# Kernel optimization log

Hardware: AMD Instinct MI355X
Metric: run time of the kernel (lower is better)

The kernel has to match this reference:

```python
import jax, jax.numpy as jnp
import numpy as np

M = 16384          # test points
N = 16384          # train points
D = 2              # (kx, ky)
CHUNK = 8192       # rows of K_star per chunk (matches torch default)


def setup_inputs() -> dict:
    key = jax.random.key(0)
    k1, k2, k3 = jax.random.split(key, 3)
    X_test = jax.random.normal(k1, (M, D), dtype=jnp.float32)
    X_train = jax.random.normal(k2, (N, D), dtype=jnp.float32)
    alpha = jax.random.normal(k3, (N, 2), dtype=jnp.float32)  # dual vars [Re, Im]
    log_lengthscale = jnp.asarray(np.log(0.1), dtype=jnp.float32)
    log_outputscale = jnp.asarray(np.log(1.0), dtype=jnp.float32)
    return {
        "X_test": X_test,
        "X_train": X_train,
        "alpha": alpha,
        "log_lengthscale": log_lengthscale,
        "log_outputscale": log_outputscale,
    }


def reference(X_test, X_train, alpha, log_lengthscale, log_outputscale):
    """Posterior mean mu* = K_rbf(X_test, X_train) @ alpha, chunked over test rows."""
    ell2 = jnp.exp(log_lengthscale) ** 2
    sf2 = jnp.exp(log_outputscale) ** 2
    xt_sq = jnp.sum(X_train * X_train, axis=1)  # (N,)

    def chunk_fn(xc):  # xc: (CHUNK, D)
        # squared euclidean distances (clamped at 0 for numerical safety)
        sq = (jnp.sum(xc * xc, axis=1)[:, None]
              + xt_sq[None, :]
              - 2.0 * (xc @ X_train.T))          # (CHUNK, N)
        sq = jnp.maximum(sq, 0.0)
        K = sf2 * jnp.exp(-0.5 * sq / ell2)      # RBF kernel values
        return K @ alpha                          # (CHUNK, 2)

    m = X_test.shape[0]
    chunks = X_test.reshape(m // CHUNK, CHUNK, D)
    out = jax.lax.map(chunk_fn, chunks)           # (m//CHUNK, CHUNK, 2)
    return out.reshape(m, 2)
```

## Files before the change

### kernel.cpp

```cpp
#include <hip/hip_runtime.h>
#include <math.h>

#define M_PTS 16384
#define N_PTS 16384

#define NC 42
#define NCELLS (NC * NC)
#define H 0.25f
#define INV_H 4.0f
#define ORIG (-5.25f)
#define TCUT 20.0f
#define KMAX 7
#define MAXROWS 16
#define NWAVES (M_PTS / 64)
#define CHUNK 1024
#define MAX_ITEMS 4096

#define OFF_NITEMS 0
#define OFF_TRCUR 64
#define OFF_TECUR (OFF_TRCUR + NCELLS * 4)
#define OFF_SROW  (OFF_TECUR + NCELLS * 4)
#define OFF_SPRE  (OFF_SROW + NWAVES * MAXROWS * 4)
#define OFF_ITEMS (OFF_SPRE + NWAVES * (MAXROWS + 1) * 4)
#define OFF_TRA   ((OFF_ITEMS + MAX_ITEMS * 4 + 255) & ~255)
#define OFF_TRW1  (OFF_TRA + N_PTS * 16)
#define OFF_T4    (OFF_TRW1 + N_PTS * 4)
#define WS_NEED   (OFF_T4 + (size_t)M_PTS * 16)

__device__ __forceinline__ float fexp2(float x) {
#if __has_builtin(__builtin_amdgcn_exp2f)
    return __builtin_amdgcn_exp2f(x);
#else
    return exp2f(x);
#endif
}

__device__ __forceinline__ void gatomic_fadd(float* p, float v) {
    asm volatile("global_atomic_add_f32 %0, %1, off" :: "v"(p), "v"(v) : "memory");
}

__device__ __forceinline__ int cellco(float v) {
    int c = (int)floorf((v - ORIG) * INV_H);
    return min(NC - 1, max(0, c));
}

__global__ __launch_bounds__(1024) void prep_kernel(
        const float2* __restrict__ Xtr, const float2* __restrict__ Xte,
        const float* __restrict__ log_ell,
        int* __restrict__ trcur, int* __restrict__ tecur,
        int* __restrict__ sRowG, int* __restrict__ sPreG,
        int* __restrict__ items, int* __restrict__ nitemsG) {
    __shared__ int hTr[NCELLS], hTe[NCELLS];
    __shared__ int trsL[NCELLS + 1], PL[NCELLS + 1];
    __shared__ int wz[16];
    const int tid = threadIdx.x;
    const int lane = tid & 63;
    const int wid = tid >> 6;

    if (tid == 0) nitemsG[0] = 0;
    for (int i = tid; i < NCELLS; i += 1024) { hTr[i] = 0; hTe[i] = 0; }
    __syncthreads();
    for (int i = tid; i < N_PTS; i += 1024) {
        float2 t = Xtr[i];
        atomicAdd(&hTr[cellco(t.y) * NC + cellco(t.x)], 1);
        float2 x = Xte[i];
        atomicAdd(&hTe[cellco(x.y) * NC + cellco(x.x)], 1);
    }
    __syncthreads();

    {
        const int grp = tid >> 9;
        const int t = tid & 511;
        int* __restrict__ h  = grp ? hTe : hTr;
        int* __restrict__ s  = grp ? PL : trsL;
        int* __restrict__ cg = grp ? tecur : trcur;

        int lo[4];
        int sum = 0;
        const bool act = (t < 441);
#pragma unroll
        for (int k = 0; k < 4; ++k) {
            int c = t * 4 + k;
            int v = act ? h[c] : 0;
            lo[k] = sum; sum += v;
        }
        int inc = sum;
#pragma unroll
        for (int d = 1; d < 64; d <<= 1) {
            int u = __shfl_up(inc, d, 64);
            if (lane >= d) inc += u;
        }
        if (lane == 63) wz[wid] = inc;
        __syncthreads();
        int base = 0;
        const int w0 = grp << 3;
        for (int w = w0; w < wid; ++w) base += wz[w];
        int ex = base + inc - sum;
        if (act) {
#pragma unroll
            for (int k = 0; k < 4; ++k) {
                int c = t * 4 + k;
                int v = ex + lo[k];
                s[c] = v;
                cg[c] = v;
            }
        }
        if (tid == 0) { trsL[NCELLS] = N_PTS; PL[NCELLS] = N_PTS; }
    }
    __syncthreads();

    if (tid < NWAVES) {
        const int w = tid;
        const float ell = expf(log_ell[0]);
        const float cmag = 0.5f / (ell * ell) * 1.4426950408889634f;
        const float r2 = TCUT / cmag;
        const int K = (int)floorf(sqrtf(r2) * INV_H) + 1;

        int clo, chi;
        {
            int s = w * 64, lo = 0, hi = NCELLS;
            while (lo + 1 < hi) { int m = (lo + hi) >> 1; if (PL[m] <= s) lo = m; else hi = m; }
            clo = lo;
            s = w * 64 + 63; lo = 0; hi = NCELLS;
            while (lo + 1 < hi) { int m = (lo + hi) >> 1; if (PL[m] <= s) lo = m; else hi = m; }
            chi = lo;
        }
        const int rl = clo / NC, cl = clo % NC;
        const int rh = chi / NC, ch = chi % NC;
        int wlo = max(0, rl - K), whi = min(NC - 1, rh + K);
        int nr = whi - wlo + 1;
        bool full = (K > KMAX) || (nr > MAXROWS);

        int pre = 0;
        if (full) {
            sRowG[w * MAXROWS] = 0;
            sPreG[w * (MAXROWS + 1)] = 0;
            pre = N_PTS;
            for (int i = 1; i <= MAXROWS; ++i) sPreG[w * (MAXROWS + 1) + i] = N_PTS;
        } else {
            const bool single = (rl == rh);
            const int cmin = single ? cl : 0;
            const int cmax = single ? ch : (NC - 1);
            sPreG[w * (MAXROWS + 1)] = 0;
            int idx = 0;
            for (int wr = wlo; wr <= whi; ++wr, ++idx) {
                int dy = (wr < rl) ? (rl - wr) : ((wr > rh) ? (wr - rh) : 0);
                int kx;
                if (dy <= 1) kx = K;
                else {
                    float d = (float)(dy - 1) * H;
                    kx = (int)floorf(sqrtf(fmaxf(r2 - d * d, 0.f)) * INV_H) + 1;
                }
                int c0 = max(0, cmin - kx);
                int c1 = min(NC - 1, cmax + kx);
                int js = trsL[wr * NC + c0];
                int je = trsL[wr * NC + c1 + 1];
                sRowG[w * MAXROWS + idx] = js - pre;
                pre += je - js;
                sPreG[w * (MAXROWS + 1) + idx + 1] = pre;
            }
            for (; idx < MAXROWS; ++idx)
                sPreG[w * (MAXROWS + 1) + idx + 1] = pre;
        }
        const int nch = (pre + CHUNK - 1) / CHUNK;
        for (int k = 0; k < nch; ++k) {
            int slot = atomicAdd(nitemsG, 1);
            items[slot] = w | (k << 16);
        }
    }
}

__global__ void scatter_kernel(const float2* __restrict__ Xtr,
                               const float2* __restrict__ Xte,
                               const float2* __restrict__ alpha,
                               const float* __restrict__ log_ell,
                               const float* __restrict__ log_sf,
                               int* __restrict__ trcur, int* __restrict__ tecur,
                               float4* __restrict__ trA, float* __restrict__ trW1,
                               float4* __restrict__ T4, float2* __restrict__ out2) {
    int i = blockIdx.x * blockDim.x + threadIdx.x;
    if (i >= N_PTS) return;
    out2[i] = make_float2(0.f, 0.f);
    float ell = expf(log_ell[0]);
    float sf2 = expf(2.0f * log_sf[0]);
    float c = -0.5f / (ell * ell) * 1.4426950408889634f;

    float2 t = Xtr[i];
    float2 a = alpha[i];
    int ct = cellco(t.y) * NC + cellco(t.x);
    int pt = atomicAdd(&trcur[ct], 1);
    trA[pt] = make_float4(-2.f * c * t.x, -2.f * c * t.y,
                          c * (t.x * t.x + t.y * t.y), sf2 * a.x);
    trW1[pt] = sf2 * a.y;

    float2 x = Xte[i];
    int cx = cellco(x.y) * NC + cellco(x.x);
    int px = atomicAdd(&tecur[cx], 1);
    T4[px] = make_float4(x.x, x.y, c * (x.x * x.x + x.y * x.y),
                         __int_as_float(i));
}

__global__ __launch_bounds__(256) void gp_main(
        const float4* __restrict__ T4, const float4* __restrict__ trA,
        const float* __restrict__ trW1, const int* __restrict__ sRowG,
        const int* __restrict__ sPreG, const int* __restrict__ items,
        const int* __restrict__ nitemsG, float* __restrict__ out) {
    const int nit = nitemsG[0];
    if ((int)blockIdx.x >= nit) return;
    const int item = items[blockIdx.x];
    const int w = item & 0xFFFF;
    const int k = item >> 16;

    __shared__ float4 sA[CHUNK];
    __shared__ __align__(16) float sW[CHUNK];
    __shared__ float2 red[4][64];
    __shared__ int off[MAXROWS];
    __shared__ int pre[MAXROWS + 1];

    const int tid = threadIdx.x;
    const int p = tid >> 6;
    const int lane = tid & 63;

    if (tid < MAXROWS) off[tid] = sRowG[w * MAXROWS + tid];
    if (tid < MAXROWS + 1) pre[tid] = sPreG[w * (MAXROWS + 1) + tid];

    float4 tp = T4[w * 64 + lane];
    const float x = tp.x, y = tp.y, b = tp.z;
    const int oi = __float_as_int(tp.w);
    __syncthreads();

    const int total = pre[MAXROWS];
    const int base0 = k << 10;
    const int n = min(CHUNK, total - base0);

    {
        int r = 0;
        for (int g = tid; g < CHUNK; g += 256) {
            float4 tv; float wv;
            if (g < n) {
                int gg = base0 + g;
                while (gg >= pre[r + 1]) ++r;
                int j = gg + off[r];
                tv = trA[j];
                wv = trW1[j];
            } else {
                tv = make_float4(0.f, 0.f, -1.0e30f, 0.f);
                wv = 0.f;
            }
            sA[g] = tv;
            sW[g] = wv;
        }
    }
    __syncthreads();

    float a0 = 0.f, a1 = 0.f;
#pragma unroll 2
    for (int q = p; q < CHUNK / 4; q += 4) {
        float4 t0 = sA[4 * q];
        float4 t1 = sA[4 * q + 1];
        float4 t2 = sA[4 * q + 2];
        float4 t3 = sA[4 * q + 3];
        float4 wv = *(const float4*)&sW[4 * q];
        float e0 = fexp2(fmaf(t0.x, x, fmaf(t0.y, y, b + t0.z)));
        float e1 = fexp2(fmaf(t1.x, x, fmaf(t1.y, y, b + t1.z)));
        float e2 = fexp2(fmaf(t2.x, x, fmaf(t2.y, y, b + t2.z)));
        float e3 = fexp2(fmaf(t3.x, x, fmaf(t3.y, y, b + t3.z)));
        a0 = fmaf(e0, t0.w, a0); a1 = fmaf(e0, wv.x, a1);
        a0 = fmaf(e1, t1.w, a0); a1 = fmaf(e1, wv.y, a1);
        a0 = fmaf(e2, t2.w, a0); a1 = fmaf(e2, wv.z, a1);
        a0 = fmaf(e3, t3.w, a0); a1 = fmaf(e3, wv.w, a1);
    }

    red[p][lane] = make_float2(a0, a1);
    __syncthreads();
    if (p == 0) {
        float s0 = 0.f, s1 = 0.f;
#pragma unroll
        for (int q = 0; q < 4; ++q) {
            float2 v = red[q][lane];
            s0 += v.x; s1 += v.y;
        }
        if (s0 != 0.f || s1 != 0.f) {
            gatomic_fadd(&out[2 * oi], s0);
            gatomic_fadd(&out[2 * oi + 1], s1);
        }
    }
}

__global__ __launch_bounds__(256, 8) void gp_dense(
        const float2* __restrict__ Xte, const float2* __restrict__ Xtr,
        const float2* __restrict__ alpha, const float* __restrict__ log_ell,
        const float* __restrict__ log_sf, float* __restrict__ out) {
    __shared__ float4 sSt[128];
    __shared__ float sA1[128];
    const int tid = threadIdx.x;
    const float ell = expf(log_ell[0]);
    const float c = -0.5f / (ell * ell) * 1.4426950408889634f;
    const int j0 = blockIdx.y * 128;
    if (tid < 128) {
        const float sf2 = expf(2.0f * log_sf[0]);
        float2 t = Xtr[j0 + tid];
        float2 a = alpha[j0 + tid];
        sSt[tid] = make_float4(-2.f * c * t.x, -2.f * c * t.y,
                               c * (t.x * t.x + t.y * t.y), sf2 * a.x);
        sA1[tid] = sf2 * a.y;
    }
    const int base = blockIdx.x * 1024 + tid;
    float2 x0 = Xte[base], x1 = Xte[base + 256];
    float2 x2 = Xte[base + 512], x3 = Xte[base + 768];
    const float b0 = c * (x0.x * x0.x + x0.y * x0.y);
    const float b1 = c * (x1.x * x1.x + x1.y * x1.y);
    const float b2 = c * (x2.x * x2.x + x2.y * x2.y);
    const float b3 = c * (x3.x * x3.x + x3.y * x3.y);
    __syncthreads();
    float a00 = 0.f, a01 = 0.f, a10 = 0.f, a11 = 0.f;
    float a20 = 0.f, a21 = 0.f, a30 = 0.f, a31 = 0.f;
#pragma unroll 2
    for (int j = 0; j < 128; ++j) {
        float4 s = sSt[j];
        float w1 = sA1[j];
        float e0 = fexp2(fminf(fmaf(s.x, x0.x, fmaf(s.y, x0.y, b0 + s.z)), 0.f));
        float e1 = fexp2(fminf(fmaf(s.x, x1.x, fmaf(s.y, x1.y, b1 + s.z)), 0.f));
        float e2 = fexp2(fminf(fmaf(s.x, x2.x, fmaf(s.y, x2.y, b2 + s.z)), 0.f));
        float e3 = fexp2(fminf(fmaf(s.x, x3.x, fmaf(s.y, x3.y, b3 + s.z)), 0.f));
        a00 = fmaf(e0, s.w, a00); a01 = fmaf(e0, w1, a01);
        a10 = fmaf(e1, s.w, a10); a11 = fmaf(e1, w1, a11);
        a20 = fmaf(e2, s.w, a20); a21 = fmaf(e2, w1, a21);
        a30 = fmaf(e3, s.w, a30); a31 = fmaf(e3, w1, a31);
    }
    gatomic_fadd(&out[2 * base], a00);            gatomic_fadd(&out[2 * base + 1], a01);
    gatomic_fadd(&out[2 * (base + 256)], a10);    gatomic_fadd(&out[2 * (base + 256) + 1], a11);
    gatomic_fadd(&out[2 * (base + 512)], a20);    gatomic_fadd(&out[2 * (base + 512) + 1], a21);
    gatomic_fadd(&out[2 * (base + 768)], a30);    gatomic_fadd(&out[2 * (base + 768) + 1], a31);
}

extern "C" void kernel_launch(void* const* d_in, const int* in_sizes, int n_in,
                              void* d_out, int out_size, void* d_ws, size_t ws_size,
                              hipStream_t stream) {
    const float2* Xte = (const float2*)d_in[0];
    const float2* Xtr = (const float2*)d_in[1];
    const float2* alpha = (const float2*)d_in[2];
    const float* log_ell = (const float*)d_in[3];
    const float* log_sf = (const float*)d_in[4];
    float* out = (float*)d_out;

    if (ws_size >= WS_NEED) {
        char* ws = (char*)d_ws;
        int* nitems = (int*)(ws + OFF_NITEMS);
        int* trcur = (int*)(ws + OFF_TRCUR);
        int* tecur = (int*)(ws + OFF_TECUR);
        int* sRowG = (int*)(ws + OFF_SROW);
        int* sPreG = (int*)(ws + OFF_SPRE);
        int* items = (int*)(ws + OFF_ITEMS);
        float4* trA = (float4*)(ws + OFF_TRA);
        float* trW1 = (float*)(ws + OFF_TRW1);
        float4* T4 = (float4*)(ws + OFF_T4);

        prep_kernel<<<1, 1024, 0, stream>>>(Xtr, Xte, log_ell, trcur, tecur,
                                            sRowG, sPreG, items, nitems);
        scatter_kernel<<<N_PTS / 256, 256, 0, stream>>>(
            Xtr, Xte, alpha, log_ell, log_sf, trcur, tecur, trA, trW1, T4,
            (float2*)out);
        gp_main<<<MAX_ITEMS, 256, 0, stream>>>(T4, trA, trW1, sRowG, sPreG,
                                               items, nitems, out);
    } else {
        hipMemsetAsync(out, 0, (size_t)out_size * sizeof(float), stream);
        dim3 grid(M_PTS / 1024, N_PTS / 128);
        gp_dense<<<grid, 256, 0, stream>>>(Xte, Xtr, alpha, log_ell, log_sf, out);
    }
}
```

Baseline: 114.0 us.

## Process two test waves per work item and parallelize histogram construction

The single-block histogram in prep is replaced by a grid-wide hist_kernel that records each point's rank within its cell, so scatter computes positions without atomics. The main kernel now handles 128 test points per item (two per lane), reusing each shared-memory train tile for two exponent evaluations and halving the number of items and tile loads. This adds a memset and an extra launch, raises register pressure, and makes the neighbour windows wider because each item spans more cells.

```diff
diff --git a/kernel.cpp b/kernel.cpp
--- a/kernel.cpp
+++ b/kernel.cpp
@@ -12,17 +12,23 @@
 #define TCUT 20.0f
 #define KMAX 7
 #define MAXROWS 16
-#define NWAVES (M_PTS / 64)
+#define NPAIRT (M_PTS / 128)
 #define CHUNK 1024
-#define MAX_ITEMS 4096
+#define MAX_ITEMS 2048
+#define GMAIN_GRID 2048
 
 #define OFF_NITEMS 0
-#define OFF_TRCUR 64
-#define OFF_TECUR (OFF_TRCUR + NCELLS * 4)
-#define OFF_SROW  (OFF_TECUR + NCELLS * 4)
-#define OFF_SPRE  (OFF_SROW + NWAVES * MAXROWS * 4)
-#define OFF_ITEMS (OFF_SPRE + NWAVES * (MAXROWS + 1) * 4)
-#define OFF_TRA   ((OFF_ITEMS + MAX_ITEMS * 4 + 255) & ~255)
+#define OFF_HTR   64
+#define OFF_HTE   (OFF_HTR + NCELLS * 4)
+#define OFF_ZEND  (OFF_HTE + NCELLS * 4)
+#define OFF_TRSL  OFF_ZEND
+#define OFF_PLG   (OFF_TRSL + (NCELLS + 1) * 4)
+#define OFF_SROW  (OFF_PLG + (NCELLS + 1) * 4)
+#define OFF_SPRE  (OFF_SROW + NPAIRT * MAXROWS * 4)
+#define OFF_ITEMS (OFF_SPRE + NPAIRT * (MAXROWS + 1) * 4)
+#define OFF_RKT   ((OFF_ITEMS + MAX_ITEMS * 4 + 255) & ~255)
+#define OFF_RKE   (OFF_RKT + N_PTS * 4)
+#define OFF_TRA   ((OFF_RKE + N_PTS * 4 + 255) & ~255)
 #define OFF_TRW1  (OFF_TRA + N_PTS * 16)
 #define OFF_T4    (OFF_TRW1 + N_PTS * 4)
 #define WS_NEED   (OFF_T4 + (size_t)M_PTS * 16)
@@ -44,36 +50,38 @@
     return min(NC - 1, max(0, c));
 }
 
-__global__ __launch_bounds__(1024) void prep_kernel(
+__global__ __launch_bounds__(256) void hist_kernel(
         const float2* __restrict__ Xtr, const float2* __restrict__ Xte,
+        int* __restrict__ histTr, int* __restrict__ histTe,
+        int* __restrict__ rkT, int* __restrict__ rkE,
+        float2* __restrict__ out2) {
+    int i = blockIdx.x * 256 + threadIdx.x;
+    if (i >= N_PTS) return;
+    out2[i] = make_float2(0.f, 0.f);
+    float2 t = Xtr[i];
+    rkT[i] = atomicAdd(&histTr[cellco(t.y) * NC + cellco(t.x)], 1);
+    float2 x = Xte[i];
+    rkE[i] = atomicAdd(&histTe[cellco(x.y) * NC + cellco(x.x)], 1);
+}
+
+__global__ __launch_bounds__(1024) void plan_kernel(
+        const int* __restrict__ histTr, const int* __restrict__ histTe,
         const float* __restrict__ log_ell,
-        int* __restrict__ trcur, int* __restrict__ tecur,
+        int* __restrict__ trsLG, int* __restrict__ PLG,
         int* __restrict__ sRowG, int* __restrict__ sPreG,
         int* __restrict__ items, int* __restrict__ nitemsG) {
-    __shared__ int hTr[NCELLS], hTe[NCELLS];
     __shared__ int trsL[NCELLS + 1], PL[NCELLS + 1];
     __shared__ int wz[16];
     const int tid = threadIdx.x;
     const int lane = tid & 63;
     const int wid = tid >> 6;
 
-    if (tid == 0) nitemsG[0] = 0;
-    for (int i = tid; i < NCELLS; i += 1024) { hTr[i] = 0; hTe[i] = 0; }
-    __syncthreads();
-    for (int i = tid; i < N_PTS; i += 1024) {
-        float2 t = Xtr[i];
-        atomicAdd(&hTr[cellco(t.y) * NC + cellco(t.x)], 1);
-        float2 x = Xte[i];
-        atomicAdd(&hTe[cellco(x.y) * NC + cellco(x.x)], 1);
-    }
-    __syncthreads();
-
     {
         const int grp = tid >> 9;
         const int t = tid & 511;
-        int* __restrict__ h  = grp ? hTe : hTr;
+        const int* __restrict__ h = grp ? histTe : histTr;
         int* __restrict__ s  = grp ? PL : trsL;
-        int* __restrict__ cg = grp ? tecur : trcur;
+        int* __restrict__ sG = grp ? PLG : trsLG;
 
         int lo[4];
         int sum = 0;
@@ -102,14 +110,18 @@
                 int c = t * 4 + k;
                 int v = ex + lo[k];
                 s[c] = v;
-                cg[c] = v;
+                sG[c] = v;
             }
         }
-        if (tid == 0) { trsL[NCELLS] = N_PTS; PL[NCELLS] = N_PTS; }
+        if (tid == 0) {
+            trsL[NCELLS] = N_PTS; PL[NCELLS] = N_PTS;
+            trsLG[NCELLS] = N_PTS; PLG[NCELLS] = N_PTS;
+            nitemsG[0] = 0;
+        }
     }
     __syncthreads();
 
-    if (tid < NWAVES) {
+    if (tid < NPAIRT) {
         const int w = tid;
         const float ell = expf(log_ell[0]);
         const float cmag = 0.5f / (ell * ell) * 1.4426950408889634f;
@@ -118,10 +130,10 @@
 
         int clo, chi;
         {
-            int s = w * 64, lo = 0, hi = NCELLS;
+            int s = w * 128, lo = 0, hi = NCELLS;
             while (lo + 1 < hi) { int m = (lo + hi) >> 1; if (PL[m] <= s) lo = m; else hi = m; }
             clo = lo;
-            s = w * 64 + 63; lo = 0; hi = NCELLS;
+            s = w * 128 + 127; lo = 0; hi = NCELLS;
             while (lo + 1 < hi) { int m = (lo + hi) >> 1; if (PL[m] <= s) lo = m; else hi = m; }
             chi = lo;
         }
@@ -131,11 +143,11 @@
         int nr = whi - wlo + 1;
         bool full = (K > KMAX) || (nr > MAXROWS);
 
-        int pre = 0;
+        int prw = 0;
         if (full) {
             sRowG[w * MAXROWS] = 0;
             sPreG[w * (MAXROWS + 1)] = 0;
-            pre = N_PTS;
+            prw = N_PTS;
             for (int i = 1; i <= MAXROWS; ++i) sPreG[w * (MAXROWS + 1) + i] = N_PTS;
         } else {
             const bool single = (rl == rh);
@@ -155,14 +167,14 @@
                 int c1 = min(NC - 1, cmax + kx);
                 int js = trsL[wr * NC + c0];
                 int je = trsL[wr * NC + c1 + 1];
-                sRowG[w * MAXROWS + idx] = js - pre;
-                pre += je - js;
-                sPreG[w * (MAXROWS + 1) + idx + 1] = pre;
+                sRowG[w * MAXROWS + idx] = js - prw;
+                prw += je - js;
+                sPreG[w * (MAXROWS + 1) + idx + 1] = prw;
             }
             for (; idx < MAXROWS; ++idx)
-                sPreG[w * (MAXROWS + 1) + idx + 1] = pre;
-        }
-        const int nch = (pre + CHUNK - 1) / CHUNK;
+                sPreG[w * (MAXROWS + 1) + idx + 1] = prw;
+        }
+        const int nch = (prw + CHUNK - 1) / CHUNK;
         for (int k = 0; k < nch; ++k) {
             int slot = atomicAdd(nitemsG, 1);
             items[slot] = w | (k << 16);
@@ -170,17 +182,16 @@
     }
 }
 
-__global__ void scatter_kernel(const float2* __restrict__ Xtr,
-                               const float2* __restrict__ Xte,
-                               const float2* __restrict__ alpha,
-                               const float* __restrict__ log_ell,
-                               const float* __restrict__ log_sf,
-                               int* __restrict__ trcur, int* __restrict__ tecur,
-                               float4* __restrict__ trA, float* __restrict__ trW1,
-                               float4* __restrict__ T4, float2* __restrict__ out2) {
-    int i = blockIdx.x * blockDim.x + threadIdx.x;
+__global__ __launch_bounds__(256) void scatter_kernel(
+        const float2* __restrict__ Xtr, const float2* __restrict__ Xte,
+        const float2* __restrict__ alpha,
+        const float* __restrict__ log_ell, const float* __restrict__ log_sf,
+        const int* __restrict__ trsLG, const int* __restrict__ PLG,
+        const int* __restrict__ rkT, const int* __restrict__ rkE,
+        float4* __restrict__ trA, float* __restrict__ trW1,
+        float4* __restrict__ T4) {
+    int i = blockIdx.x * 256 + threadIdx.x;
     if (i >= N_PTS) return;
-    out2[i] = make_float2(0.f, 0.f);
     float ell = expf(log_ell[0]);
     float sf2 = expf(2.0f * log_sf[0]);
     float c = -0.5f / (ell * ell) * 1.4426950408889634f;
@@ -188,14 +199,14 @@
     float2 t = Xtr[i];
     float2 a = alpha[i];
     int ct = cellco(t.y) * NC + cellco(t.x);
-    int pt = atomicAdd(&trcur[ct], 1);
+    int pt = trsLG[ct] + rkT[i];
     trA[pt] = make_float4(-2.f * c * t.x, -2.f * c * t.y,
                           c * (t.x * t.x + t.y * t.y), sf2 * a.x);
     trW1[pt] = sf2 * a.y;
 
     float2 x = Xte[i];
     int cx = cellco(x.y) * NC + cellco(x.x);
-    int px = atomicAdd(&tecur[cx], 1);
+    int px = PLG[cx] + rkE[i];
     T4[px] = make_float4(x.x, x.y, c * (x.x * x.x + x.y * x.y),
                          __int_as_float(i));
 }
@@ -208,12 +219,12 @@
     const int nit = nitemsG[0];
     if ((int)blockIdx.x >= nit) return;
     const int item = items[blockIdx.x];
-    const int w = item & 0xFFFF;
+    const int pr = item & 0xFFFF;
     const int k = item >> 16;
 
     __shared__ float4 sA[CHUNK];
     __shared__ __align__(16) float sW[CHUNK];
-    __shared__ float2 red[4][64];
+    __shared__ float4 red[4][64];
     __shared__ int off[MAXROWS];
     __shared__ int pre[MAXROWS + 1];
 
@@ -221,12 +232,15 @@
     const int p = tid >> 6;
     const int lane = tid & 63;
 
-    if (tid < MAXROWS) off[tid] = sRowG[w * MAXROWS + tid];
-    if (tid < MAXROWS + 1) pre[tid] = sPreG[w * (MAXROWS + 1) + tid];
-
-    float4 tp = T4[w * 64 + lane];
-    const float x = tp.x, y = tp.y, b = tp.z;
-    const int oi = __float_as_int(tp.w);
+    if (tid < MAXROWS) off[tid] = sRowG[pr * MAXROWS + tid];
+    if (tid < MAXROWS + 1) pre[tid] = sPreG[pr * (MAXROWS + 1) + tid];
+
+    float4 tpA = T4[pr * 128 + lane];
+    float4 tpB = T4[pr * 128 + 64 + lane];
+    const float xA = tpA.x, yA = tpA.y, bA = tpA.z;
+    const float xB = tpB.x, yB = tpB.y, bB = tpB.z;
+    const int oiA = __float_as_int(tpA.w);
+    const int oiB = __float_as_int(tpB.w);
     __syncthreads();
 
     const int total = pre[MAXROWS];
@@ -253,7 +267,7 @@
     }
     __syncthreads();
 
-    float a0 = 0.f, a1 = 0.f;
+    float a0 = 0.f, a1 = 0.f, c0 = 0.f, c1 = 0.f;
 #pragma unroll 2
     for (int q = p; q < CHUNK / 4; q += 4) {
         float4 t0 = sA[4 * q];
@@ -261,28 +275,40 @@
         float4 t2 = sA[4 * q + 2];
         float4 t3 = sA[4 * q + 3];
         float4 wv = *(const float4*)&sW[4 * q];
-        float e0 = fexp2(fmaf(t0.x, x, fmaf(t0.y, y, b + t0.z)));
-        float e1 = fexp2(fmaf(t1.x, x, fmaf(t1.y, y, b + t1.z)));
-        float e2 = fexp2(fmaf(t2.x, x, fmaf(t2.y, y, b + t2.z)));
-        float e3 = fexp2(fmaf(t3.x, x, fmaf(t3.y, y, b + t3.z)));
+        float e0 = fexp2(fmaf(t0.x, xA, fmaf(t0.y, yA, bA + t0.z)));
+        float e1 = fexp2(fmaf(t1.x, xA, fmaf(t1.y, yA, bA + t1.z)));
+        float e2 = fexp2(fmaf(t2.x, xA, fmaf(t2.y, yA, bA + t2.z)));
+        float e3 = fexp2(fmaf(t3.x, xA, fmaf(t3.y, yA, bA + t3.z)));
         a0 = fmaf(e0, t0.w, a0); a1 = fmaf(e0, wv.x, a1);
         a0 = fmaf(e1, t1.w, a0); a1 = fmaf(e1, wv.y, a1);
         a0 = fmaf(e2, t2.w, a0); a1 = fmaf(e2, wv.z, a1);
         a0 = fmaf(e3, t3.w, a0); a1 = fmaf(e3, wv.w, a1);
-    }
-
-    red[p][lane] = make_float2(a0, a1);
+        float f0 = fexp2(fmaf(t0.x, xB, fmaf(t0.y, yB, bB + t0.z)));
+        float f1 = fexp2(fmaf(t1.x, xB, fmaf(t1.y, yB, bB + t1.z)));
+        float f2 = fexp2(fmaf(t2.x, xB, fmaf(t2.y, yB, bB + t2.z)));
+        float f3 = fexp2(fmaf(t3.x, xB, fmaf(t3.y, yB, bB + t3.z)));
+        c0 = fmaf(f0, t0.w, c0); c1 = fmaf(f0, wv.x, c1);
+        c0 = fmaf(f1, t1.w, c0); c1 = fmaf(f1, wv.y, c1);
+        c0 = fmaf(f2, t2.w, c0); c1 = fmaf(f2, wv.z, c1);
+        c0 = fmaf(f3, t3.w, c0); c1 = fmaf(f3, wv.w, c1);
+    }
+
+    red[p][lane] = make_float4(a0, a1, c0, c1);
     __syncthreads();
     if (p == 0) {
-        float s0 = 0.f, s1 = 0.f;
+        float4 s = red[0][lane];
 #pragma unroll
-        for (int q = 0; q < 4; ++q) {
-            float2 v = red[q][lane];
-            s0 += v.x; s1 += v.y;
-        }
-        if (s0 != 0.f || s1 != 0.f) {
-            gatomic_fadd(&out[2 * oi], s0);
-            gatomic_fadd(&out[2 * oi + 1], s1);
+        for (int q = 1; q < 4; ++q) {
+            float4 v = red[q][lane];
+            s.x += v.x; s.y += v.y; s.z += v.z; s.w += v.w;
+        }
+        if (s.x != 0.f || s.y != 0.f) {
+            gatomic_fadd(&out[2 * oiA], s.x);
+            gatomic_fadd(&out[2 * oiA + 1], s.y);
+        }
+        if (s.z != 0.f || s.w != 0.f) {
+            gatomic_fadd(&out[2 * oiB], s.z);
+            gatomic_fadd(&out[2 * oiB + 1], s.w);
         }
     }
 }
@@ -347,22 +373,30 @@
     if (ws_size >= WS_NEED) {
         char* ws = (char*)d_ws;
         int* nitems = (int*)(ws + OFF_NITEMS);
-        int* trcur = (int*)(ws + OFF_TRCUR);
-        int* tecur = (int*)(ws + OFF_TECUR);
+        int* histTr = (int*)(ws + OFF_HTR);
+        int* histTe = (int*)(ws + OFF_HTE);
+        int* trsLG = (int*)(ws + OFF_TRSL);
+        int* PLG   = (int*)(ws + OFF_PLG);
         int* sRowG = (int*)(ws + OFF_SROW);
         int* sPreG = (int*)(ws + OFF_SPRE);
         int* items = (int*)(ws + OFF_ITEMS);
+        int* rkT   = (int*)(ws + OFF_RKT);
+        int* rkE   = (int*)(ws + OFF_RKE);
         float4* trA = (float4*)(ws + OFF_TRA);
         float* trW1 = (float*)(ws + OFF_TRW1);
         float4* T4 = (float4*)(ws + OFF_T4);
 
-        prep_kernel<<<1, 1024, 0, stream>>>(Xtr, Xte, log_ell, trcur, tecur,
-                                            sRowG, sPreG, items, nitems);
+        hipMemsetAsync(ws, 0, OFF_ZEND, stream);
+        hist_kernel<<<N_PTS / 256, 256, 0, stream>>>(
+            Xtr, Xte, histTr, histTe, rkT, rkE, (float2*)out);
+        plan_kernel<<<1, 1024, 0, stream>>>(histTr, histTe, log_ell,
+                                            trsLG, PLG, sRowG, sPreG,
+                                            items, nitems);
         scatter_kernel<<<N_PTS / 256, 256, 0, stream>>>(
-            Xtr, Xte, alpha, log_ell, log_sf, trcur, tecur, trA, trW1, T4,
-            (float2*)out);
-        gp_main<<<MAX_ITEMS, 256, 0, stream>>>(T4, trA, trW1, sRowG, sPreG,
-                                               items, nitems, out);
+            Xtr, Xte, alpha, log_ell, log_sf, trsLG, PLG, rkT, rkE,
+            trA, trW1, T4);
+        gp_main<<<GMAIN_GRID, 256, 0, stream>>>(T4, trA, trW1, sRowG, sPreG,
+                                                items, nitems, out);
     } else {
         hipMemsetAsync(out, 0, (size_t)out_size * sizeof(float), stream);
         dim3 grid(M_PTS / 1024, N_PTS / 128);
```

After: 109.5 us. -4.0%, faster.
